# Performance work log

Hardware: AMD Instinct MI355X
Metric: run time of the kernel (lower is better)

The kernel has to match this reference:

```python
import jax, jax.numpy as jnp
import numpy as np
import math

D_MODEL = 1024
NUM_HEADS = 16
D_FF = 4096
EPS = 1e-5


def _linear_params(key, fan_in, fan_out):
    # torch nn.Linear default init: U(-1/sqrt(fan_in), 1/sqrt(fan_in))
    k1, k2 = jax.random.split(key)
    bound = 1.0 / math.sqrt(fan_in)
    W = jax.random.uniform(k1, (fan_in, fan_out), jnp.float32, -bound, bound)
    b = jax.random.uniform(k2, (fan_out,), jnp.float32, -bound, bound)
    return W, b


def setup_inputs() -> dict:
    key = jax.random.key(0)
    keys = jax.random.split(key, 16)
    src = jax.random.normal(keys[0], (4, 2048, D_MODEL), jnp.float32)
    tgt = jax.random.normal(keys[1], (4, 2048, D_MODEL), jnp.float32)
    sa_wq, sa_bq = _linear_params(keys[2], D_MODEL, D_MODEL)
    sa_wk, sa_bk = _linear_params(keys[3], D_MODEL, D_MODEL)
    sa_wv, sa_bv = _linear_params(keys[4], D_MODEL, D_MODEL)
    sa_wo, sa_bo = _linear_params(keys[5], D_MODEL, D_MODEL)
    ca_wq, ca_bq = _linear_params(keys[6], D_MODEL, D_MODEL)
    ca_wk, ca_bk = _linear_params(keys[7], D_MODEL, D_MODEL)
    ca_wv, ca_bv = _linear_params(keys[8], D_MODEL, D_MODEL)
    ca_wo, ca_bo = _linear_params(keys[9], D_MODEL, D_MODEL)
    ff_w1, ff_b1 = _linear_params(keys[10], D_MODEL, D_FF)
    ff_w2, ff_b2 = _linear_params(keys[11], D_FF, D_MODEL)
    ones = jnp.ones((D_MODEL,), jnp.float32)
    zeros = jnp.zeros((D_MODEL,), jnp.float32)
    return dict(
        src=src, tgt=tgt,
        sa_wq=sa_wq, sa_bq=sa_bq, sa_wk=sa_wk, sa_bk=sa_bk,
        sa_wv=sa_wv, sa_bv=sa_bv, sa_wo=sa_wo, sa_bo=sa_bo,
        ca_wq=ca_wq, ca_bq=ca_bq, ca_wk=ca_wk, ca_bk=ca_bk,
        ca_wv=ca_wv, ca_bv=ca_bv, ca_wo=ca_wo, ca_bo=ca_bo,
        ff_w1=ff_w1, ff_b1=ff_b1, ff_w2=ff_w2, ff_b2=ff_b2,
        ln1_g=ones, ln1_b=zeros, ln2_g=ones, ln2_b=zeros,
        ln3_g=ones, ln3_b=zeros,
    )


def _layernorm(x, g, b):
    mu = jnp.mean(x, axis=-1, keepdims=True)
    var = jnp.mean((x - mu) ** 2, axis=-1, keepdims=True)
    return (x - mu) * jax.lax.rsqrt(var + EPS) * g + b


def _mha(q_in, kv_in, wq, bq, wk, bk, wv, bv, wo, bo):
    B, Sq, D = q_in.shape
    Skv = kv_in.shape[1]
    H, dk = NUM_HEADS, D // NUM_HEADS
    Q = (q_in @ wq + bq).reshape(B, Sq, H, dk).transpose(0, 2, 1, 3)
    K = (kv_in @ wk + bk).reshape(B, Skv, H, dk).transpose(0, 2, 1, 3)
    V = (kv_in @ wv + bv).reshape(B, Skv, H, dk).transpose(0, 2, 1, 3)
    scores = jnp.einsum('bhqd,bhkd->bhqk', Q, K) / math.sqrt(dk)
    probs = jax.nn.softmax(scores, axis=-1)
    attn = jnp.einsum('bhqk,bhkd->bhqd', probs, V)
    attn = attn.transpose(0, 2, 1, 3).reshape(B, Sq, D)
    return attn @ wo + bo


def reference(src, tgt,
              sa_wq, sa_bq, sa_wk, sa_bk, sa_wv, sa_bv, sa_wo, sa_bo,
              ca_wq, ca_bq, ca_wk, ca_bk, ca_wv, ca_bv, ca_wo, ca_bo,
              ff_w1, ff_b1, ff_w2, ff_b2,
              ln1_g, ln1_b, ln2_g, ln2_b, ln3_g, ln3_b):
    # self-attention on tgt (dropout = identity in eval)
    sa = _mha(tgt, tgt, sa_wq, sa_bq, sa_wk, sa_bk, sa_wv, sa_bv, sa_wo, sa_bo)
    x = _layernorm(tgt + sa, ln1_g, ln1_b)
    # cross-attention: queries from decoder, keys/values from src
    ca = _mha(x, src, ca_wq, ca_bq, ca_wk, ca_bk, ca_wv, ca_bv, ca_wo, ca_bo)
    x = _layernorm(x + ca, ln2_g, ln2_b)
    # feed-forward
    ff = jax.nn.relu(x @ ff_w1 + ff_b1) @ ff_w2 + ff_b2
    x = _layernorm(x + ff, ln3_g, ln3_b)
    return x
```

## Files before the change

### kernel.cpp

```cpp
#include <hip/hip_runtime.h>
#include <hip/hip_bf16.h>
#include <stdint.h>


typedef __bf16 bf16_t;
typedef __bf16 bf16x8 __attribute__((ext_vector_type(8)));
typedef __bf16 bf16x4 __attribute__((ext_vector_type(4)));
typedef float  f32x4  __attribute__((ext_vector_type(4)));
typedef short  s16x4  __attribute__((ext_vector_type(4)));

#define SEQ_    2048
#define BATCH_  4
#define DM_     1024
#define NH_     16
#define DK_     64
#define DFF_    4096
#define TOK_    (BATCH_*SEQ_)
#define BH_     (BATCH_*NH_)
#define HEADEL_ ((size_t)BH_*SEQ_*DK_)

#define QSCALE_ 0.18033688011112042f

#define MFMA_BF16(a,b,c) __builtin_amdgcn_mfma_f32_16x16x32_bf16((a),(b),(c),0,0,0)
#define MFMA16(a,b,c) __builtin_amdgcn_mfma_f32_16x16x16bf16_1k((a),(b),(c),0,0,0)

static __device__ __forceinline__ void gl_lds16(const void* g, void* l) {
  __builtin_amdgcn_global_load_lds(
      (const __attribute__((address_space(1))) uint32_t*)g,
      (__attribute__((address_space(3))) uint32_t*)l, 16, 0, 0);
}

static __device__ __forceinline__ float fast_exp2(float x) {
#if __has_builtin(__builtin_amdgcn_exp2f)
  return __builtin_amdgcn_exp2f(x);
#else
  return exp2f(x);
#endif
}

__global__ __launch_bounds__(256) void cvt_bf16(const float* __restrict__ in,
                                                bf16_t* __restrict__ out, int n4) {
  int i = blockIdx.x * 256 + threadIdx.x;
  if (i < n4) {
    f32x4 v = *(const f32x4*)(in + (size_t)i * 4);
    bf16x4 o;
    o[0] = (bf16_t)v[0]; o[1] = (bf16_t)v[1]; o[2] = (bf16_t)v[2]; o[3] = (bf16_t)v[3];
    *(bf16x4*)(out + (size_t)i * 4) = o;
  }
}

__global__ __launch_bounds__(256) void transpose_w(const float* __restrict__ W,
                                                   bf16_t* __restrict__ Wt,
                                                   int K, int N) {
  __shared__ float t[32][33];
  int bx = blockIdx.x * 32;
  int by = blockIdx.y * 32;
  int tx = threadIdx.x;
  int ty = threadIdx.y;
  #pragma unroll
  for (int i = 0; i < 32; i += 8)
    t[ty + i][tx] = W[(size_t)(by + ty + i) * N + bx + tx];
  __syncthreads();
  #pragma unroll
  for (int i = 0; i < 32; i += 8)
    Wt[(size_t)(bx + ty + i) * K + by + tx] = (bf16_t)t[tx][ty + i];
}

__global__ __launch_bounds__(256) void transpose_w8(
    const float* __restrict__ w0, const float* __restrict__ w1,
    const float* __restrict__ w2, const float* __restrict__ w3,
    const float* __restrict__ w4, const float* __restrict__ w5,
    const float* __restrict__ w6, const float* __restrict__ w7,
    bf16_t* __restrict__ dst)
{
  __shared__ float t[32][33];
  const int z = blockIdx.z;
  const float* W;
  switch (z) {
    case 0: W = w0; break; case 1: W = w1; break;
    case 2: W = w2; break; case 3: W = w3; break;
    case 4: W = w4; break; case 5: W = w5; break;
    case 6: W = w6; break; default: W = w7; break;
  }
  bf16_t* Wt = dst + (size_t)z * DM_ * DM_;
  int bx = blockIdx.x * 32;
  int by = blockIdx.y * 32;
  int tx = threadIdx.x;
  int ty = threadIdx.y;
  #pragma unroll
  for (int i = 0; i < 32; i += 8)
    t[ty + i][tx] = W[(size_t)(by + ty + i) * DM_ + bx + tx];
  __syncthreads();
  #pragma unroll
  for (int i = 0; i < 32; i += 8)
    Wt[(size_t)(bx + ty + i) * DM_ + by + tx] = (bf16_t)t[tx][ty + i];
}

__global__ __launch_bounds__(256) void gemm_bf16(
    const bf16_t* __restrict__ A, const bf16_t* __restrict__ Bt,
    const float* __restrict__ bias, const float* __restrict__ bias2,
    const float* __restrict__ bias3,
    float* outF, float* outF2, bf16_t* outB,
    int M, int N, int K, int mode, int relu, float scale, int ksplit)
{
  __shared__ __attribute__((aligned(16))) bf16_t lsA[2][128 * 32];
  __shared__ __attribute__((aligned(16))) bf16_t lsB[2][128 * 32];

  const int tid  = threadIdx.x;
  const int lane = tid & 63;
  const int w    = tid >> 6;
  const int q    = lane >> 4;
  const int r    = lane & 15;

  const int gx = gridDim.x;
  const int b  = blockIdx.y * gx + blockIdx.x;
  const int t_ = b >> 3;
  int bm = (t_ / gx) * 8 + (b & 7);
  const int bn = t_ % gx;

  int kidx = 0;
  int kbeg = 0, kend = K;
  if (ksplit == 2) {
    const int mtiles = M >> 7;
    if (bm >= mtiles) { kidx = 1; bm -= mtiles; }
    const int kh = K >> 1;
    kbeg = kidx * kh; kend = kbeg + kh;
  }
  const int m0 = bm * 128;
  const int n0 = bn * 128;

  const int mb   = (w >> 1) * 64;
  const int nb   = (w & 1) * 64;

  f32x4 acc[4][4] = {};

  for (int k0 = kbeg; k0 < kend; k0 += 64) {
    #pragma unroll
    for (int h = 0; h < 2; ++h) {
      #pragma unroll
      for (int rr = 0; rr < 2; ++rr) {
        int flat = rr * 2048 + tid * 8;
        int row = flat >> 5, col = flat & 31;
        gl_lds16(A  + (size_t)(m0 + row) * K + k0 + 32 * h + col, &lsA[h][flat]);
        gl_lds16(Bt + (size_t)(n0 + row) * K + k0 + 32 * h + col, &lsB[h][flat]);
      }
    }
    __syncthreads();
    #pragma unroll
    for (int h = 0; h < 2; ++h) {
      bf16x8 af[4], bfr[4];
      #pragma unroll
      for (int mi = 0; mi < 4; ++mi)
        af[mi] = *(const bf16x8*)&lsA[h][(mb + mi * 16 + r) * 32 + q * 8];
      #pragma unroll
      for (int ni = 0; ni < 4; ++ni)
        bfr[ni] = *(const bf16x8*)&lsB[h][(nb + ni * 16 + r) * 32 + q * 8];
      #pragma unroll
      for (int mi = 0; mi < 4; ++mi)
        #pragma unroll
        for (int ni = 0; ni < 4; ++ni)
          acc[mi][ni] = MFMA_BF16(af[mi], bfr[ni], acc[mi][ni]);
    }
    __syncthreads();
  }

  float* ofp = kidx ? outF2 : outF;

  #pragma unroll
  for (int mi = 0; mi < 4; ++mi) {
    #pragma unroll
    for (int ni = 0; ni < 4; ++ni) {
      int col = n0 + nb + ni * 16 + r;
      float bv, sc = scale;
      int seg = 0, cw = col;
      if (mode == 3) {
        seg = col >> 10; cw = col & 1023;
        bv = (seg == 0) ? bias[cw] : ((seg == 1) ? bias2[cw] : bias3[cw]);
        if (seg != 0) sc = 1.f;
      } else if (mode == 4) {
        seg = col >> 10; cw = col & 1023;
        bv = (seg == 0) ? bias[cw] : bias2[cw];
      } else {
        bv = bias[col];
      }
      if (kidx) bv = 0.f;
      #pragma unroll
      for (int i = 0; i < 4; ++i) {
        int row = m0 + mb + mi * 16 + q * 4 + i;
        float v = (acc[mi][ni][i] + bv) * sc;
        if (relu) v = fmaxf(v, 0.f);
        if (ofp) ofp[(size_t)row * N + col] = v;
        if (outB) {
          size_t idx;
          if (mode == 0) {
            idx = (size_t)row * N + col;
          } else {
            int bb = row >> 11, s = row & 2047, h = cw >> 6, d = cw & 63;
            bool vt;
            size_t base;
            if (mode == 1)      { vt = false; base = 0; }
            else if (mode == 2) { vt = true;  base = 0; }
            else if (mode == 3) { vt = (seg == 2); base = (size_t)seg * HEADEL_; }
            else                { vt = (seg == 1); base = (size_t)seg * HEADEL_; }
            if (!vt) idx = base + ((size_t)(bb * NH_ + h) * SEQ_ + s) * DK_ + d;
            else     idx = base + ((size_t)(bb * NH_ + h) * DK_ + d) * SEQ_ + s;
          }
          outB[idx] = (bf16_t)v;
        }
      }
    }
  }
}

__global__ __launch_bounds__(256) void flash_attn(
    const bf16_t* __restrict__ Q, const bf16_t* __restrict__ Kb,
    const bf16_t* __restrict__ Vt, bf16_t* __restrict__ O)
{
  __shared__ __attribute__((aligned(16))) bf16_t Kls[64 * 64];
  __shared__ __attribute__((aligned(16))) bf16_t Vls[64 * 64];

  const int tid  = threadIdx.x;
  const int w    = tid >> 6;
  const int lane = tid & 63;
  const int q    = lane >> 4;
  const int r    = lane & 15;

  const int bl   = blockIdx.y * gridDim.x + blockIdx.x;
  const int bh   = (bl & 7) * 8 + ((bl >> 3) & 7);
  const int q0   = (bl >> 6) * 128 + w * 32;

  const bf16_t* Qp  = Q  + ((size_t)bh * SEQ_ + q0) * DK_;
  const bf16_t* Kp0 = Kb + (size_t)bh * SEQ_ * DK_;
  const bf16_t* Vp0 = Vt + (size_t)bh * DK_ * SEQ_;

  bf16x8 aq[2][2];
  #pragma unroll
  for (int rt = 0; rt < 2; ++rt)
    #pragma unroll
    for (int c = 0; c < 2; ++c)
      aq[rt][c] = *(const bf16x8*)(Qp + (rt * 16 + r) * DK_ + 32 * c + 8 * q);

  f32x4 o[2][4] = {};
  f32x4 l4[2] = {};

  const int srow0 = tid >> 3;
  const int scol0 = ((tid & 7) ^ (srow0 & 7)) * 8;
  const int srow1 = srow0 + 32;
  const int scol1 = ((tid & 7) ^ (srow1 & 7)) * 8;
  const int r7 = r & 7;

  for (int kv = 0; kv < SEQ_; kv += 64) {
    gl_lds16(Kp0 + (size_t)(kv + srow0) * DK_ + scol0, Kls + tid * 8);
    gl_lds16(Kp0 + (size_t)(kv + srow1) * DK_ + scol1, Kls + 2048 + tid * 8);
    gl_lds16(Vp0 + (size_t)srow0 * SEQ_ + kv + scol0, Vls + tid * 8);
    gl_lds16(Vp0 + (size_t)srow1 * SEQ_ + kv + scol1, Vls + 2048 + tid * 8);
    __syncthreads();

    bf16x8 kf[4][2];
    #pragma unroll
    for (int mt = 0; mt < 4; ++mt)
      #pragma unroll
      for (int c = 0; c < 2; ++c)
        kf[mt][c] = *(const bf16x8*)&Kls[(((16 * mt + r) * 8) + ((4 * c + q) ^ r7)) * 8];
    s16x4 vf[4][4];
    #pragma unroll
    for (int dt = 0; dt < 4; ++dt)
      #pragma unroll
      for (int mt = 0; mt < 4; ++mt)
        vf[dt][mt] = *(const s16x4*)&Vls[(((16 * dt + r) * 8) +
                        ((2 * mt + (q >> 1)) ^ r7)) * 8 + (q & 1) * 4];

    #pragma unroll
    for (int rt = 0; rt < 2; ++rt) {
      f32x4 st[4] = {};
      #pragma unroll
      for (int mt = 0; mt < 4; ++mt) {
        st[mt] = MFMA_BF16(kf[mt][0], aq[rt][0], st[mt]);
        st[mt] = MFMA_BF16(kf[mt][1], aq[rt][1], st[mt]);
      }
      s16x4 pf[4];
      f32x4 psum = {};
      #pragma unroll
      for (int mt = 0; mt < 4; ++mt) {
        f32x4 pe;
        #pragma unroll
        for (int i = 0; i < 4; ++i) pe[i] = fast_exp2(st[mt][i]);
        psum += pe;
        bf16x4 pb;
        #pragma unroll
        for (int i = 0; i < 4; ++i) pb[i] = (bf16_t)pe[i];
        pf[mt] = __builtin_bit_cast(s16x4, pb);
      }
      l4[rt] += psum;
      #pragma unroll
      for (int dt = 0; dt < 4; ++dt)
        #pragma unroll
        for (int mt = 0; mt < 4; ++mt)
          o[rt][dt] = MFMA16(vf[dt][mt], pf[mt], o[rt][dt]);
    }
    __syncthreads();
  }

  const int b = bh >> 4, h = bh & 15;
  #pragma unroll
  for (int rt = 0; rt < 2; ++rt) {
    float lr = (l4[rt][0] + l4[rt][1]) + (l4[rt][2] + l4[rt][3]);
    lr += __shfl_xor(lr, 16);
    lr += __shfl_xor(lr, 32);
    float linv = 1.f / lr;
    int token = b * SEQ_ + q0 + rt * 16 + r;
    #pragma unroll
    for (int dt = 0; dt < 4; ++dt) {
      bf16x4 ob;
      #pragma unroll
      for (int i = 0; i < 4; ++i) ob[i] = (bf16_t)(o[rt][dt][i] * linv);
      *(bf16x4*)(O + (size_t)token * DM_ + h * DK_ + 16 * dt + 4 * q) = ob;
    }
  }
}

__global__ __launch_bounds__(256) void resid_ln(
    const float* A, const float* Bv, const float* Cv,
    const float* g, const float* be,
    float* outF, bf16_t* outB)
{
  const int w = threadIdx.x >> 6, lane = threadIdx.x & 63;
  const int row = blockIdx.x * 4 + w;
  const float* a = A  + (size_t)row * DM_;
  const float* b = Bv + (size_t)row * DM_;
  const float* c3 = Cv ? Cv + (size_t)row * DM_ : nullptr;
  float v[16];
  float s = 0.f;
  #pragma unroll
  for (int c = 0; c < 4; ++c) {
    f32x4 x = *(const f32x4*)(a + c * 256 + lane * 4);
    f32x4 y = *(const f32x4*)(b + c * 256 + lane * 4);
    f32x4 z = {};
    if (c3) z = *(const f32x4*)(c3 + c * 256 + lane * 4);
    #pragma unroll
    for (int k = 0; k < 4; ++k) {
      v[c * 4 + k] = x[k] + y[k] + z[k];
      s += v[c * 4 + k];
    }
  }
  s += __shfl_xor(s, 1);  s += __shfl_xor(s, 2);  s += __shfl_xor(s, 4);
  s += __shfl_xor(s, 8);  s += __shfl_xor(s, 16); s += __shfl_xor(s, 32);
  float mu = s * (1.f / DM_);
  float ss = 0.f;
  #pragma unroll
  for (int k = 0; k < 16; ++k) { float d = v[k] - mu; ss += d * d; }
  ss += __shfl_xor(ss, 1);  ss += __shfl_xor(ss, 2);  ss += __shfl_xor(ss, 4);
  ss += __shfl_xor(ss, 8);  ss += __shfl_xor(ss, 16); ss += __shfl_xor(ss, 32);
  float rstd = rsqrtf(ss * (1.f / DM_) + 1e-5f);
  #pragma unroll
  for (int c = 0; c < 4; ++c) {
    int idx = c * 256 + lane * 4;
    f32x4 gg = *(const f32x4*)(g + idx);
    f32x4 bb = *(const f32x4*)(be + idx);
    f32x4 ov; bf16x4 ob;
    #pragma unroll
    for (int k = 0; k < 4; ++k) {
      float val = (v[c * 4 + k] - mu) * rstd * gg[k] + bb[k];
      ov[k] = val; ob[k] = (bf16_t)val;
    }
    *(f32x4*)(outF + (size_t)row * DM_ + idx) = ov;
    if (outB) *(bf16x4*)(outB + (size_t)row * DM_ + idx) = ob;
  }
}

extern "C" void kernel_launch(void* const* d_in, const int* in_sizes, int n_in,
                              void* d_out, int out_size, void* d_ws, size_t ws_size,
                              hipStream_t stream)
{
  (void)in_sizes; (void)n_in; (void)out_size; (void)ws_size;
  const float* src   = (const float*)d_in[0];
  const float* tgt   = (const float*)d_in[1];
  const float* sa_wq = (const float*)d_in[2];  const float* sa_bq = (const float*)d_in[3];
  const float* sa_wk = (const float*)d_in[4];  const float* sa_bk = (const float*)d_in[5];
  const float* sa_wv = (const float*)d_in[6];  const float* sa_bv = (const float*)d_in[7];
  const float* sa_wo = (const float*)d_in[8];  const float* sa_bo = (const float*)d_in[9];
  const float* ca_wq = (const float*)d_in[10]; const float* ca_bq = (const float*)d_in[11];
  const float* ca_wk = (const float*)d_in[12]; const float* ca_bk = (const float*)d_in[13];
  const float* ca_wv = (const float*)d_in[14]; const float* ca_bv = (const float*)d_in[15];
  const float* ca_wo = (const float*)d_in[16]; const float* ca_bo = (const float*)d_in[17];
  const float* ff_w1 = (const float*)d_in[18]; const float* ff_b1 = (const float*)d_in[19];
  const float* ff_w2 = (const float*)d_in[20]; const float* ff_b2 = (const float*)d_in[21];
  const float* ln1g  = (const float*)d_in[22]; const float* ln1b  = (const float*)d_in[23];
  const float* ln2g  = (const float*)d_in[24]; const float* ln2b  = (const float*)d_in[25];
  const float* ln3g  = (const float*)d_in[26]; const float* ln3b  = (const float*)d_in[27];

  char* p = (char*)d_ws;
  auto alloc = [&](size_t bytes) -> char* {
    char* r = p; p += (bytes + 255) & ~(size_t)255; return r;
  };

  const size_t ACT_B  = (size_t)TOK_ * DM_ * 2;
  const size_t W_B    = (size_t)DM_ * DM_ * 2;
  const size_t HEAD_B = HEADEL_ * 2;

  bf16_t* tgt_bf = (bf16_t*)alloc(ACT_B);
  bf16_t* src_bf = (bf16_t*)alloc(ACT_B);
  bf16_t* wt_saq = (bf16_t*)alloc(W_B);
  bf16_t* wt_sak = (bf16_t*)alloc(W_B);
  bf16_t* wt_sav = (bf16_t*)alloc(W_B);
  bf16_t* wt_sao = (bf16_t*)alloc(W_B);
  bf16_t* wt_caq = (bf16_t*)alloc(W_B);
  bf16_t* wt_cak = (bf16_t*)alloc(W_B);
  bf16_t* wt_cav = (bf16_t*)alloc(W_B);
  bf16_t* wt_cao = (bf16_t*)alloc(W_B);
  bf16_t* w1t    = (bf16_t*)alloc((size_t)DFF_ * DM_ * 2);
  bf16_t* w2t    = (bf16_t*)alloc((size_t)DM_ * DFF_ * 2);
  char*   Rg     = alloc((size_t)TOK_ * DFF_ * 2);
  bf16_t* Qb     = (bf16_t*)Rg;
  bf16_t* Kbuf   = (bf16_t*)(Rg + HEAD_B);
  bf16_t* Vtb    = (bf16_t*)(Rg + 2 * HEAD_B);
  bf16_t* attnO  = (bf16_t*)(Rg + 3 * HEAD_B);
  bf16_t* hbuf   = (bf16_t*)Rg;
  float*  x1F    = (float*)alloc((size_t)TOK_ * DM_ * 4);
  bf16_t* x1B    = (bf16_t*)alloc(ACT_B);
  float*  x2F    = (float*)alloc((size_t)TOK_ * DM_ * 4);
  bf16_t* x2B    = (bf16_t*)alloc(ACT_B);
  float*  yF     = (float*)d_out;

  const int n4 = TOK_ * DM_ / 4;
  cvt_bf16<<<n4 / 256, 256, 0, stream>>>(tgt, tgt_bf, n4);
  cvt_bf16<<<n4 / 256, 256, 0, stream>>>(src, src_bf, n4);

  dim3 tb(32, 8);
  transpose_w8<<<dim3(32, 32, 8), tb, 0, stream>>>(
      sa_wq, sa_wk, sa_wv, sa_wo, ca_wq, ca_wk, ca_wv, ca_wo, wt_saq);
  transpose_w<<<dim3(128, 32), tb, 0, stream>>>(ff_w1, w1t, DM_, DFF_);
  transpose_w<<<dim3(32, 128), tb, 0, stream>>>(ff_w2, w2t, DFF_, DM_);

  dim3 g1(DM_ / 128, TOK_ / 128);
  dim3 g3(3 * DM_ / 128, TOK_ / 128);
  dim3 g2(2 * DM_ / 128, TOK_ / 128);
  dim3 gf(DFF_ / 128, TOK_ / 128);
  dim3 gs(DM_ / 128, 2 * TOK_ / 128);
  dim3 ga(SEQ_ / 128, BH_);

  gemm_bf16<<<g3, 256, 0, stream>>>(tgt_bf, wt_saq, sa_bq, sa_bk, sa_bv,
                                    nullptr, nullptr, Qb,
                                    TOK_, 3 * DM_, DM_, 3, 0, QSCALE_, 1);
  flash_attn<<<ga, 256, 0, stream>>>(Qb, Kbuf, Vtb, attnO);
  gemm_bf16<<<g1, 256, 0, stream>>>(attnO, wt_sao, sa_bo, nullptr, nullptr,
                                    yF, nullptr, nullptr,
                                    TOK_, DM_, DM_, 0, 0, 1.f, 1);
  resid_ln<<<TOK_ / 4, 256, 0, stream>>>(tgt, yF, nullptr, ln1g, ln1b, x1F, x1B);

  gemm_bf16<<<g1, 256, 0, stream>>>(x1B, wt_caq, ca_bq, nullptr, nullptr,
                                    nullptr, nullptr, Qb,
                                    TOK_, DM_, DM_, 1, 0, QSCALE_, 1);
  gemm_bf16<<<g2, 256, 0, stream>>>(src_bf, wt_cak, ca_bk, ca_bv, nullptr,
                                    nullptr, nullptr, Kbuf,
                                    TOK_, 2 * DM_, DM_, 4, 0, 1.f, 1);
  flash_attn<<<ga, 256, 0, stream>>>(Qb, Kbuf, Vtb, attnO);
  gemm_bf16<<<g1, 256, 0, stream>>>(attnO, wt_cao, ca_bo, nullptr, nullptr,
                                    yF, nullptr, nullptr,
                                    TOK_, DM_, DM_, 0, 0, 1.f, 1);
  resid_ln<<<TOK_ / 4, 256, 0, stream>>>(x1F, yF, nullptr, ln2g, ln2b, x2F, x2B);

  gemm_bf16<<<gf, 256, 0, stream>>>(x2B, w1t, ff_b1, nullptr, nullptr,
                                    nullptr, nullptr, hbuf,
                                    TOK_, DFF_, DM_, 0, 1, 1.f, 1);
  gemm_bf16<<<gs, 256, 0, stream>>>(hbuf, w2t, ff_b2, nullptr, nullptr,
                                    yF, x1F, nullptr,
                                    TOK_, DM_, DFF_, 0, 0, 1.f, 2);
  resid_ln<<<TOK_ / 4, 256, 0, stream>>>(x2F, yF, x1F,
                                         ln3g, ln3b, (float*)d_out, nullptr);
}
```

Baseline: 968.0 us.

## Swizzle GEMM LDS tiles and drop split-K for the FFN down-projection

```diff
diff --git a/kernel.cpp b/kernel.cpp
--- a/kernel.cpp
+++ b/kernel.cpp
@@ -100,8 +100,8 @@
     const bf16_t* __restrict__ A, const bf16_t* __restrict__ Bt,
     const float* __restrict__ bias, const float* __restrict__ bias2,
     const float* __restrict__ bias3,
-    float* outF, float* outF2, bf16_t* outB,
-    int M, int N, int K, int mode, int relu, float scale, int ksplit)
+    float* outF, bf16_t* outB,
+    int M, int N, int K, int mode, int relu, float scale)
 {
   __shared__ __attribute__((aligned(16))) bf16_t lsA[2][128 * 32];
   __shared__ __attribute__((aligned(16))) bf16_t lsB[2][128 * 32];
@@ -115,32 +115,26 @@
   const int gx = gridDim.x;
   const int b  = blockIdx.y * gx + blockIdx.x;
   const int t_ = b >> 3;
-  int bm = (t_ / gx) * 8 + (b & 7);
+  const int bm = (t_ / gx) * 8 + (b & 7);
   const int bn = t_ % gx;
-
-  int kidx = 0;
-  int kbeg = 0, kend = K;
-  if (ksplit == 2) {
-    const int mtiles = M >> 7;
-    if (bm >= mtiles) { kidx = 1; bm -= mtiles; }
-    const int kh = K >> 1;
-    kbeg = kidx * kh; kend = kbeg + kh;
-  }
   const int m0 = bm * 128;
   const int n0 = bn * 128;
 
   const int mb   = (w >> 1) * 64;
   const int nb   = (w & 1) * 64;
 
+  const int qs = (q ^ ((r >> 1) & 3)) * 8;
+
   f32x4 acc[4][4] = {};
 
-  for (int k0 = kbeg; k0 < kend; k0 += 64) {
+  for (int k0 = 0; k0 < K; k0 += 64) {
     #pragma unroll
     for (int h = 0; h < 2; ++h) {
       #pragma unroll
       for (int rr = 0; rr < 2; ++rr) {
         int flat = rr * 2048 + tid * 8;
-        int row = flat >> 5, col = flat & 31;
+        int row  = flat >> 5;
+        int col  = ((((flat >> 3) & 3) ^ ((flat >> 6) & 3)) << 3);
         gl_lds16(A  + (size_t)(m0 + row) * K + k0 + 32 * h + col, &lsA[h][flat]);
         gl_lds16(Bt + (size_t)(n0 + row) * K + k0 + 32 * h + col, &lsB[h][flat]);
       }
@@ -151,10 +145,10 @@
       bf16x8 af[4], bfr[4];
       #pragma unroll
       for (int mi = 0; mi < 4; ++mi)
-        af[mi] = *(const bf16x8*)&lsA[h][(mb + mi * 16 + r) * 32 + q * 8];
+        af[mi] = *(const bf16x8*)&lsA[h][(mb + mi * 16 + r) * 32 + qs];
       #pragma unroll
       for (int ni = 0; ni < 4; ++ni)
-        bfr[ni] = *(const bf16x8*)&lsB[h][(nb + ni * 16 + r) * 32 + q * 8];
+        bfr[ni] = *(const bf16x8*)&lsB[h][(nb + ni * 16 + r) * 32 + qs];
       #pragma unroll
       for (int mi = 0; mi < 4; ++mi)
         #pragma unroll
@@ -163,8 +157,6 @@
     }
     __syncthreads();
   }
-
-  float* ofp = kidx ? outF2 : outF;
 
   #pragma unroll
   for (int mi = 0; mi < 4; ++mi) {
@@ -183,13 +175,12 @@
       } else {
         bv = bias[col];
       }
-      if (kidx) bv = 0.f;
       #pragma unroll
       for (int i = 0; i < 4; ++i) {
         int row = m0 + mb + mi * 16 + q * 4 + i;
         float v = (acc[mi][ni][i] + bv) * sc;
         if (relu) v = fmaxf(v, 0.f);
-        if (ofp) ofp[(size_t)row * N + col] = v;
+        if (outF) outF[(size_t)row * N + col] = v;
         if (outB) {
           size_t idx;
           if (mode == 0) {
@@ -436,36 +427,28 @@
   dim3 g3(3 * DM_ / 128, TOK_ / 128);
   dim3 g2(2 * DM_ / 128, TOK_ / 128);
   dim3 gf(DFF_ / 128, TOK_ / 128);
-  dim3 gs(DM_ / 128, 2 * TOK_ / 128);
   dim3 ga(SEQ_ / 128, BH_);
 
   gemm_bf16<<<g3, 256, 0, stream>>>(tgt_bf, wt_saq, sa_bq, sa_bk, sa_bv,
-                                    nullptr, nullptr, Qb,
-                                    TOK_, 3 * DM_, DM_, 3, 0, QSCALE_, 1);
+                                    nullptr, Qb, TOK_, 3 * DM_, DM_, 3, 0, QSCALE_);
   flash_attn<<<ga, 256, 0, stream>>>(Qb, Kbuf, Vtb, attnO);
   gemm_bf16<<<g1, 256, 0, stream>>>(attnO, wt_sao, sa_bo, nullptr, nullptr,
-                                    yF, nullptr, nullptr,
-                                    TOK_, DM_, DM_, 0, 0, 1.f, 1);
+                                    yF, nullptr, TOK_, DM_, DM_, 0, 0, 1.f);
   resid_ln<<<TOK_ / 4, 256, 0, stream>>>(tgt, yF, nullptr, ln1g, ln1b, x1F, x1B);
 
   gemm_bf16<<<g1, 256, 0, stream>>>(x1B, wt_caq, ca_bq, nullptr, nullptr,
-                                    nullptr, nullptr, Qb,
-                                    TOK_, DM_, DM_, 1, 0, QSCALE_, 1);
+                                    nullptr, Qb, TOK_, DM_, DM_, 1, 0, QSCALE_);
   gemm_bf16<<<g2, 256, 0, stream>>>(src_bf, wt_cak, ca_bk, ca_bv, nullptr,
-                                    nullptr, nullptr, Kbuf,
-                                    TOK_, 2 * DM_, DM_, 4, 0, 1.f, 1);
+                                    nullptr, Kbuf, TOK_, 2 * DM_, DM_, 4, 0, 1.f);
   flash_attn<<<ga, 256, 0, stream>>>(Qb, Kbuf, Vtb, attnO);
   gemm_bf16<<<g1, 256, 0, stream>>>(attnO, wt_cao, ca_bo, nullptr, nullptr,
-                                    yF, nullptr, nullptr,
-                                    TOK_, DM_, DM_, 0, 0, 1.f, 1);
+                                    yF, nullptr, TOK_, DM_, DM_, 0, 0, 1.f);
   resid_ln<<<TOK_ / 4, 256, 0, stream>>>(x1F, yF, nullptr, ln2g, ln2b, x2F, x2B);
 
   gemm_bf16<<<gf, 256, 0, stream>>>(x2B, w1t, ff_b1, nullptr, nullptr,
-                                    nullptr, nullptr, hbuf,
-                                    TOK_, DFF_, DM_, 0, 1, 1.f, 1);
-  gemm_bf16<<<gs, 256, 0, stream>>>(hbuf, w2t, ff_b2, nullptr, nullptr,
-                                    yF, x1F, nullptr,
-                                    TOK_, DM_, DFF_, 0, 0, 1.f, 2);
-  resid_ln<<<TOK_ / 4, 256, 0, stream>>>(x2F, yF, x1F,
-                                         ln3g, ln3b, (float*)d_out, nullptr);
-}
+                                    nullptr, hbuf, TOK_, DFF_, DM_, 0, 1, 1.f);
+  gemm_bf16<<<g1, 256, 0, stream>>>(hbuf, w2t, ff_b2, nullptr, nullptr,
+                                    yF, nullptr, TOK_, DM_, DFF_, 0, 0, 1.f);
+  resid_ln<<<TOK_ / 4, 256, 0, stream>>>(x2F, yF, nullptr, ln3g, ln3b,
+                                         (float*)d_out, nullptr);
+}
```

Result: faster. 934.8 us (-3.4%).
